# Optimization experiments

Measured on AMD Instinct MI355X. Metric: run time of the kernel, lower is better.

The kernel has to match this reference:

```python
import jax, jax.numpy as jnp
import numpy as np

B, T, C, H = 4, 4096, 1024, 64  # batch, seq, n_embd, head_size

def setup_inputs() -> dict:
    key = jax.random.key(0)
    kx, kq, kk, kv = jax.random.split(key, 4)
    x = jax.random.normal(kx, (B, T, C), dtype=jnp.float32)
    s = 1.0 / np.sqrt(C)
    Wq = jax.random.normal(kq, (C, H), dtype=jnp.float32) * s
    Wk = jax.random.normal(kk, (C, H), dtype=jnp.float32) * s
    Wv = jax.random.normal(kv, (C, H), dtype=jnp.float32) * s
    return {"x": x, "Wq": Wq, "Wk": Wk, "Wv": Wv}

def reference(x, Wq, Wk, Wv):
    B_, T_, C_ = x.shape
    q = x @ Wq  # [B,T,H]
    k = x @ Wk
    v = x @ Wv
    # NOTE: original scales by C**-0.5 (n_embd), not head_size**-0.5
    scale = jnp.asarray(C_, x.dtype) ** -0.5
    wei = jnp.einsum('bth,bsh->bts', q, k) * scale  # [B,T,T]
    causal = jnp.tril(jnp.ones((T_, T_), dtype=bool))
    wei = jnp.where(causal, wei, -jnp.inf)
    wei = jax.nn.softmax(wei, axis=-1)
    out = jnp.einsum('bts,bsh->bth', wei, v)  # [B,T,H]
    return out
```

## Files before the change

### kernel.cpp

```cpp
#include <hip/hip_runtime.h>
#include <hip/hip_bf16.h>
#include <math.h>

#define BB 4
#define TT 4096
#define CC 1024
#define HH 64

typedef __attribute__((ext_vector_type(8))) short short8;
typedef __attribute__((ext_vector_type(8))) unsigned short ushort8;
typedef __attribute__((ext_vector_type(4))) float f32x4;
typedef __attribute__((ext_vector_type(2))) unsigned int uint2v;
typedef __attribute__((ext_vector_type(4))) unsigned int uint4v;

__device__ inline unsigned short f2bf(float f) {
    unsigned int u = __builtin_bit_cast(unsigned int, f);
    unsigned int r = u + 0x7fffu + ((u >> 16) & 1u);
    return (unsigned short)(r >> 16);
}

__device__ inline unsigned int cvtpk(float lo, float hi) {
    unsigned int r;
    asm("v_cvt_pk_bf16_f32 %0, %1, %2" : "=v"(r) : "v"(lo), "v"(hi));
    return r;
}

__device__ inline float exp2v(float x) {
    float r;
    asm("v_exp_f32 %0, %1" : "=v"(r) : "v"(x));
    return r;
}

__device__ inline void gll16(const void* g, void* l) {
    __builtin_amdgcn_global_load_lds(
        (const __attribute__((address_space(1))) unsigned int*)g,
        (__attribute__((address_space(3))) unsigned int*)l,
        16, 0, 0);
}

__device__ inline int soff_strip(int qs) {
    if (qs < 128) return (qs - 64) * 2;
    if (qs < 192) return 128 + (qs - 128) * 3;
    return 320 + (qs - 192) * 4;
}

__global__ __launch_bounds__(256) void wtrans_kernel(
    const float* __restrict__ Wq,
    const float* __restrict__ Wk,
    const float* __restrict__ Wv,
    unsigned short* __restrict__ Wf)
{
    const int t = blockIdx.x * 256 + threadIdx.x;
    const int lane = t & 63;
    const int ntl  = (t >> 6) % 12;
    const int kt   = t / 768;
    const int quad = lane >> 4, n = lane & 15;
    const int m    = ntl >> 2;
    const int col  = (ntl & 3) * 16 + n;
    const float* src = (m == 0) ? Wq : (m == 1) ? Wk : Wv;
    ushort8 u;
#pragma unroll
    for (int j = 0; j < 8; ++j)
        u[j] = f2bf(src[(kt * 32 + quad * 8 + j) * 64 + col]);
    *(ushort8*)(Wf + (size_t)t * 8) = u;
}

__global__ __launch_bounds__(512, 2) void qkv_gemm(
    const float* __restrict__ x,
    const unsigned short* __restrict__ Wf,
    unsigned short* __restrict__ Qb,
    unsigned short* __restrict__ Kf,
    unsigned short* __restrict__ Vf)
{
    __shared__ __align__(16) unsigned char smem[122880];
    float (*Tl)[200] = (float (*)[200])smem;

    const int tid  = threadIdx.x;
    const int lane = tid & 63;
    const int wave = tid >> 6;
    const int n    = lane & 15;
    const int quad = lane >> 4;
    const int mt   = wave & 3;
    const int ch   = wave >> 2;

    const int row0g = blockIdx.x * 64;
    const int b     = row0g >> 12;
    const int st    = (row0g & (TT - 1)) >> 6;

    const char* xg = (const char*)(x + (size_t)row0g * CC);
    const char* wg = (const char*)Wf;

    f32x4 acc[6];
#pragma unroll
    for (int i = 0; i < 6; ++i) acc[i] = (f32x4){0.f, 0.f, 0.f, 0.f};

    auto stage = [&](int bb, int s) {
        unsigned char* base = smem + bb * 40960;
#pragma unroll
        for (int i = 0; i < 2; ++i) {
            const int rr = (i * 8 + wave) * 4 + (lane >> 4);
            const int cb = ((lane & 15) * 16) ^ ((rr & 7) << 4);
            gll16(xg + (size_t)rr * 4096 + s * 256 + cb,
                  base + (i * 8 + wave) * 1024);
        }
#pragma unroll
        for (int i = 0; i < 3; ++i) {
            const int off = (i * 8 + wave) * 1024;
            gll16(wg + (size_t)s * 24576 + off + lane * 16,
                  base + 16384 + off);
        }
    };

    auto compute = [&](int bb) {
        const unsigned char* xb = smem + bb * 40960;
        const unsigned char* wb = xb + 16384;
        const int row = mt * 16 + n;
        const int swz = (n & 7) << 4;
#pragma unroll
        for (int ktl = 0; ktl < 2; ++ktl) {
            const int c0 = (ktl * 128 + quad * 32) ^ swz;
            const int c1 = (ktl * 128 + quad * 32 + 16) ^ swz;
            const float4 f0 = *(const float4*)(xb + row * 256 + c0);
            const float4 f1 = *(const float4*)(xb + row * 256 + c1);
            uint4v u;
            u[0] = cvtpk(f0.x, f0.y);
            u[1] = cvtpk(f0.z, f0.w);
            u[2] = cvtpk(f1.x, f1.y);
            u[3] = cvtpk(f1.z, f1.w);
            const short8 a0 = __builtin_bit_cast(short8, u);
#pragma unroll
            for (int t = 0; t < 6; ++t) {
                const int g = ch * 6 + t;
                const short8 bwv = *(const short8*)(wb + (ktl * 12 + g) * 1024 + lane * 16);
                acc[t] = __builtin_amdgcn_mfma_f32_16x16x32_bf16(a0, bwv, acc[t], 0, 0, 0);
            }
        }
    };

    stage(0, 0);
    stage(1, 1);
#pragma unroll
    for (int s = 0; s < 16; ++s) {
        if (s + 2 < 16) stage((s + 2) % 3, s + 2);
        if (s <= 13)      asm volatile("s_waitcnt vmcnt(10)" ::: "memory");
        else if (s == 14) asm volatile("s_waitcnt vmcnt(5)"  ::: "memory");
        else              asm volatile("s_waitcnt vmcnt(0)"  ::: "memory");
        __builtin_amdgcn_sched_barrier(0);
        __builtin_amdgcn_s_barrier();
        compute(s % 3);
        __builtin_amdgcn_s_barrier();
    }

#pragma unroll
    for (int t = 0; t < 6; ++t) {
        const int g   = ch * 6 + t;
        const int col = (g >> 2) * 64 + (g & 3) * 16 + n;
#pragma unroll
        for (int r = 0; r < 4; ++r)
            Tl[mt * 16 + quad * 4 + r][col] = acc[t][r];
    }
    __syncthreads();

    {
        const int row = tid & 63;
        const int c0  = (tid >> 6) * 8;
        const float qsc = 0.045084220f;
        uint4v w4;
        w4[0] = cvtpk(Tl[row][c0]     * qsc, Tl[row][c0 + 1] * qsc);
        w4[1] = cvtpk(Tl[row][c0 + 2] * qsc, Tl[row][c0 + 3] * qsc);
        w4[2] = cvtpk(Tl[row][c0 + 4] * qsc, Tl[row][c0 + 5] * qsc);
        w4[3] = cvtpk(Tl[row][c0 + 6] * qsc, Tl[row][c0 + 7] * qsc);
        *(uint4v*)(Qb + (size_t)(row0g + row) * HH + c0) = w4;
    }
    {
        const int mt2 = wave >> 1, kk = wave & 1;
        ushort8 u;
#pragma unroll
        for (int j = 0; j < 8; ++j)
            u[j] = f2bf(Tl[mt2 * 16 + n][64 + kk * 32 + quad * 8 + j]);
        const size_t r = (size_t)(((b * 64 + st) * 4 + mt2) * 2 + kk) * 64 + lane;
        *(ushort8*)(Kf + r * 8) = u;
    }
    {
        const int ht = wave >> 1, kv = wave & 1;
        ushort8 u;
#pragma unroll
        for (int j = 0; j < 8; ++j)
            u[j] = f2bf(Tl[kv * 32 + quad * 8 + j][128 + ht * 16 + n]);
        const size_t r = (size_t)(((b * 64 + st) * 4 + ht) * 2 + kv) * 64 + lane;
        *(ushort8*)(Vf + r * 8) = u;
    }
}

__global__ __launch_bounds__(256) void attn_kernel(
    const unsigned short* __restrict__ Qb,
    const unsigned short* __restrict__ Kf,
    const unsigned short* __restrict__ Vf,
    float* __restrict__ out,
    float* __restrict__ scr)
{
    __shared__ unsigned short Ps[4][2][16][76];

    const int tid  = threadIdx.x;
    const int lane = tid & 63;
    const int wave = tid >> 6;
    const int n    = lane & 15;
    const int quad = lane >> 4;

    const int wid = blockIdx.x * 4 + wave;
    const int b   = wid / 640;
    const int u   = 639 - (wid - b * 640);

    int qs, ci;
    if (u < 64)        { qs = u;                  ci = 0; }
    else if (u < 192)  { const int v = u - 64;  qs = 64  + (v >> 1); ci = v & 1; }
    else if (u < 384)  { const int v = u - 192; const int d = v / 3;
                         qs = 128 + d;            ci = v - 3 * d; }
    else               { const int v = u - 384; qs = 192 + (v >> 2); ci = v & 3; }

    const int stmax = qs >> 2;
    const int st0   = ci << 4;
    const int stEnd = min(stmax, st0 + 15);
    const int nc    = (stmax + 16) >> 4;
    const int qrow  = qs * 16 + n;

    const unsigned short* qp = Qb + ((size_t)b * TT + qrow) * HH;
    const short8 bQ0 = *(const short8*)(qp + quad * 8);
    const short8 bQ1 = *(const short8*)(qp + 32 + quad * 8);

    const unsigned short* KfB = Kf + (size_t)b * 262144;
    const unsigned short* VfB = Vf + (size_t)b * 262144;

    f32x4 O[4];
#pragma unroll
    for (int ht = 0; ht < 4; ++ht) O[ht] = (f32x4){0.f, 0.f, 0.f, 0.f};
    float l = 0.f;

    short8 kA[4], kB[4];
#pragma unroll
    for (int mt = 0; mt < 4; ++mt) {
        const unsigned short* kp = KfB + (size_t)((st0 * 4 + mt) * 2) * 512 + lane * 8;
        kA[mt] = *(const short8*)(kp);
        kB[mt] = *(const short8*)(kp + 512);
    }

    for (int st = st0; st <= stEnd; ++st) {
        f32x4 S[4];
#pragma unroll
        for (int mt = 0; mt < 4; ++mt) {
            f32x4 acc = (f32x4){0.f, 0.f, 0.f, 0.f};
            acc = __builtin_amdgcn_mfma_f32_16x16x32_bf16(kA[mt], bQ0, acc, 0, 0, 0);
            acc = __builtin_amdgcn_mfma_f32_16x16x32_bf16(kB[mt], bQ1, acc, 0, 0, 0);
            S[mt] = acc;
        }

        short8 vA[4], vB[4];
#pragma unroll
        for (int ht = 0; ht < 4; ++ht) {
            const unsigned short* vp = VfB + (size_t)((st * 4 + ht) * 2) * 512 + lane * 8;
            vA[ht] = *(const short8*)(vp);
            vB[ht] = *(const short8*)(vp + 512);
        }
        if (st < stEnd) {
#pragma unroll
            for (int mt = 0; mt < 4; ++mt) {
                const unsigned short* kp = KfB + (size_t)(((st + 1) * 4 + mt) * 2) * 512 + lane * 8;
                kA[mt] = *(const short8*)(kp);
                kB[mt] = *(const short8*)(kp + 512);
            }
        }

        if (st == stmax) {
#pragma unroll
            for (int mt = 0; mt < 4; ++mt) {
                const int sg = st * 64 + mt * 16 + quad * 4;
#pragma unroll
                for (int r = 0; r < 4; ++r)
                    if (sg + r > qrow) S[mt][r] = -INFINITY;
            }
        }

#pragma unroll
        for (int mt = 0; mt < 4; ++mt)
#pragma unroll
            for (int r = 0; r < 4; ++r) {
                const float p = exp2v(fminf(S[mt][r], 43.28085f));
                S[mt][r] = p;
                l += p;
            }

        const int pp = st & 1;
#pragma unroll
        for (int mt = 0; mt < 4; ++mt) {
            uint2v w;
            w[0] = cvtpk(S[mt][0], S[mt][1]);
            w[1] = cvtpk(S[mt][2], S[mt][3]);
            *(uint2v*)&Ps[wave][pp][n][mt * 16 + quad * 4] = w;
        }
        asm volatile("s_waitcnt lgkmcnt(0)" ::: "memory");
        const short8 bP0 = *(const short8*)&Ps[wave][pp][n][quad * 8];
        const short8 bP1 = *(const short8*)&Ps[wave][pp][n][32 + quad * 8];

#pragma unroll
        for (int ht = 0; ht < 4; ++ht) {
            O[ht] = __builtin_amdgcn_mfma_f32_16x16x32_bf16(vA[ht], bP0, O[ht], 0, 0, 0);
            O[ht] = __builtin_amdgcn_mfma_f32_16x16x32_bf16(vB[ht], bP1, O[ht], 0, 0, 0);
        }
    }

    l += __shfl_xor(l, 16);
    l += __shfl_xor(l, 32);

    if (nc == 1) {
        const float inv = 1.0f / l;
        float* op = out + ((size_t)b * TT + qrow) * HH;
#pragma unroll
        for (int ht = 0; ht < 4; ++ht) {
            float4 o4;
            o4.x = O[ht][0] * inv;
            o4.y = O[ht][1] * inv;
            o4.z = O[ht][2] * inv;
            o4.w = O[ht][3] * inv;
            *(float4*)(op + ht * 16 + quad * 4) = o4;
        }
    } else {
        float* sb = scr + (size_t)(b * 576 + soff_strip(qs) + ci) * 1040;
        float* rp = sb + n * 64;
#pragma unroll
        for (int ht = 0; ht < 4; ++ht)
            *(f32x4*)(rp + ht * 16 + quad * 4) = O[ht];
        if (quad == 0) sb[1024 + n] = l;
    }
}

__global__ __launch_bounds__(64) void combine_kernel(
    const float* __restrict__ scr,
    float* __restrict__ out)
{
    const int b  = blockIdx.x / 192;
    const int qs = 64 + blockIdx.x % 192;
    const int nc = ((qs >> 2) + 16) >> 4;
    const int base = b * 576 + soff_strip(qs);

    const int t    = threadIdx.x;
    const int row  = t >> 2;
    const int col0 = (t & 3) * 16;

    f32x4 s0 = (f32x4){0.f,0.f,0.f,0.f}, s1 = s0, s2 = s0, s3 = s0;
    float lsum = 0.f;
    for (int ci = 0; ci < nc; ++ci) {
        const float* sb = scr + (size_t)(base + ci) * 1040;
        lsum += sb[1024 + row];
        const float* p = sb + row * 64 + col0;
        s0 += *(const f32x4*)(p);
        s1 += *(const f32x4*)(p + 4);
        s2 += *(const f32x4*)(p + 8);
        s3 += *(const f32x4*)(p + 12);
    }
    const float inv = 1.0f / lsum;
    float* op = out + ((size_t)b * TT + qs * 16 + row) * HH + col0;
    *(f32x4*)(op)      = s0 * inv;
    *(f32x4*)(op + 4)  = s1 * inv;
    *(f32x4*)(op + 8)  = s2 * inv;
    *(f32x4*)(op + 12) = s3 * inv;
}

extern "C" void kernel_launch(void* const* d_in, const int* in_sizes, int n_in,
                              void* d_out, int out_size, void* d_ws, size_t ws_size,
                              hipStream_t stream)
{
    const float* x  = (const float*)d_in[0];
    const float* Wq = (const float*)d_in[1];
    const float* Wk = (const float*)d_in[2];
    const float* Wv = (const float*)d_in[3];

    unsigned short* Qb = (unsigned short*)d_ws;
    unsigned short* Wf = Qb + (size_t)BB * TT * HH;
    unsigned short* Kf = Wf + (size_t)192 * 1024;
    unsigned short* Vf = Kf + (size_t)BB * 262144;
    float*          scr = (float*)(Vf + (size_t)BB * 262144);
    float* out = (float*)d_out;

    wtrans_kernel<<<96, 256, 0, stream>>>(Wq, Wk, Wv, Wf);
    qkv_gemm<<<BB * TT / 64, 512, 0, stream>>>(x, Wf, Qb, Kf, Vf);
    attn_kernel<<<640, 256, 0, stream>>>(Qb, Kf, Vf, out, scr);
    combine_kernel<<<768, 64, 0, stream>>>(scr, out);
}
```

Measured before the change: 145.6 us.

## Software-pipeline PV MFMA of previous tile with QK and softmax of current tile

```diff
diff --git a/kernel.cpp b/kernel.cpp
--- a/kernel.cpp
+++ b/kernel.cpp
@@ -243,9 +243,9 @@
         kA[mt] = *(const short8*)(kp);
         kB[mt] = *(const short8*)(kp + 512);
     }
-
-    for (int st = st0; st <= stEnd; ++st) {
-        f32x4 S[4];
+    short8 vA[4], vB[4];
+
+    auto qk_mask_softmax_write = [&](int st, f32x4* S) {
 #pragma unroll
         for (int mt = 0; mt < 4; ++mt) {
             f32x4 acc = (f32x4){0.f, 0.f, 0.f, 0.f};
@@ -253,8 +253,13 @@
             acc = __builtin_amdgcn_mfma_f32_16x16x32_bf16(kB[mt], bQ1, acc, 0, 0, 0);
             S[mt] = acc;
         }
-
-        short8 vA[4], vB[4];
+    };
+
+    {
+        const int st = st0;
+        f32x4 S[4];
+        qk_mask_softmax_write(st, S);
+
 #pragma unroll
         for (int ht = 0; ht < 4; ++ht) {
             const unsigned short* vp = VfB + (size_t)((st * 4 + ht) * 2) * 512 + lane * 8;
@@ -269,7 +274,6 @@
                 kB[mt] = *(const short8*)(kp + 512);
             }
         }
-
         if (st == stmax) {
 #pragma unroll
             for (int mt = 0; mt < 4; ++mt) {
@@ -279,7 +283,6 @@
                     if (sg + r > qrow) S[mt][r] = -INFINITY;
             }
         }
-
 #pragma unroll
         for (int mt = 0; mt < 4; ++mt)
 #pragma unroll
@@ -288,7 +291,6 @@
                 S[mt][r] = p;
                 l += p;
             }
-
         const int pp = st & 1;
 #pragma unroll
         for (int mt = 0; mt < 4; ++mt) {
@@ -297,10 +299,68 @@
             w[1] = cvtpk(S[mt][2], S[mt][3]);
             *(uint2v*)&Ps[wave][pp][n][mt * 16 + quad * 4] = w;
         }
-        asm volatile("s_waitcnt lgkmcnt(0)" ::: "memory");
-        const short8 bP0 = *(const short8*)&Ps[wave][pp][n][quad * 8];
-        const short8 bP1 = *(const short8*)&Ps[wave][pp][n][32 + quad * 8];
-
+    }
+
+    for (int st = st0 + 1; st <= stEnd; ++st) {
+        const unsigned short* prow = &Ps[wave][(st - 1) & 1][n][0];
+        const short8 bP0 = *(const short8*)(prow + quad * 8);
+        const short8 bP1 = *(const short8*)(prow + 32 + quad * 8);
+
+        f32x4 S[4];
+        qk_mask_softmax_write(st, S);
+
+#pragma unroll
+        for (int ht = 0; ht < 4; ++ht) {
+            O[ht] = __builtin_amdgcn_mfma_f32_16x16x32_bf16(vA[ht], bP0, O[ht], 0, 0, 0);
+            O[ht] = __builtin_amdgcn_mfma_f32_16x16x32_bf16(vB[ht], bP1, O[ht], 0, 0, 0);
+        }
+
+#pragma unroll
+        for (int ht = 0; ht < 4; ++ht) {
+            const unsigned short* vp = VfB + (size_t)((st * 4 + ht) * 2) * 512 + lane * 8;
+            vA[ht] = *(const short8*)(vp);
+            vB[ht] = *(const short8*)(vp + 512);
+        }
+        if (st < stEnd) {
+#pragma unroll
+            for (int mt = 0; mt < 4; ++mt) {
+                const unsigned short* kp = KfB + (size_t)(((st + 1) * 4 + mt) * 2) * 512 + lane * 8;
+                kA[mt] = *(const short8*)(kp);
+                kB[mt] = *(const short8*)(kp + 512);
+            }
+        }
+
+        if (st == stmax) {
+#pragma unroll
+            for (int mt = 0; mt < 4; ++mt) {
+                const int sg = st * 64 + mt * 16 + quad * 4;
+#pragma unroll
+                for (int r = 0; r < 4; ++r)
+                    if (sg + r > qrow) S[mt][r] = -INFINITY;
+            }
+        }
+#pragma unroll
+        for (int mt = 0; mt < 4; ++mt)
+#pragma unroll
+            for (int r = 0; r < 4; ++r) {
+                const float p = exp2v(fminf(S[mt][r], 43.28085f));
+                S[mt][r] = p;
+                l += p;
+            }
+        const int pp = st & 1;
+#pragma unroll
+        for (int mt = 0; mt < 4; ++mt) {
+            uint2v w;
+            w[0] = cvtpk(S[mt][0], S[mt][1]);
+            w[1] = cvtpk(S[mt][2], S[mt][3]);
+            *(uint2v*)&Ps[wave][pp][n][mt * 16 + quad * 4] = w;
+        }
+    }
+
+    {
+        const unsigned short* prow = &Ps[wave][stEnd & 1][n][0];
+        const short8 bP0 = *(const short8*)(prow + quad * 8);
+        const short8 bP1 = *(const short8*)(prow + 32 + quad * 8);
 #pragma unroll
         for (int ht = 0; ht < 4; ++ht) {
             O[ht] = __builtin_amdgcn_mfma_f32_16x16x32_bf16(vA[ht], bP0, O[ht], 0, 0, 0);
```

New measurement: 144.5 us. No clear change (-0.7%).

## Share K/V tiles across block waves via LDS double buffering with software-pipelined PV

Applied to the files above, without the earlier changes.

```diff
diff --git a/kernel.cpp b/kernel.cpp
--- a/kernel.cpp
+++ b/kernel.cpp
@@ -199,6 +199,7 @@
     float* __restrict__ out,
     float* __restrict__ scr)
 {
+    __shared__ __align__(16) unsigned char kv[32768];
     __shared__ unsigned short Ps[4][2][16][76];
 
     const int tid  = threadIdx.x;
@@ -207,44 +208,76 @@
     const int n    = lane & 15;
     const int quad = lane >> 4;
 
-    const int wid = blockIdx.x * 4 + wave;
-    const int b   = wid / 640;
-    const int u   = 639 - (wid - b * 640);
-
-    int qs, ci;
-    if (u < 64)        { qs = u;                  ci = 0; }
-    else if (u < 192)  { const int v = u - 64;  qs = 64  + (v >> 1); ci = v & 1; }
-    else if (u < 384)  { const int v = u - 192; const int d = v / 3;
-                         qs = 128 + d;            ci = v - 3 * d; }
-    else               { const int v = u - 384; qs = 192 + (v >> 2); ci = v & 3; }
-
-    const int stmax = qs >> 2;
+    const int bid = blockIdx.x;
+    const int b   = bid / 160;
+    const int u   = 159 - (bid - b * 160);
+
+    int g, ci;
+    if (u < 16)       { g = u;                 ci = 0; }
+    else if (u < 48)  { const int v = u - 16;  g = 16 + (v >> 1); ci = v & 1; }
+    else if (u < 96)  { const int v = u - 48;  const int d = v / 3;
+                        g = 32 + d;            ci = v - 3 * d; }
+    else              { const int v = u - 96;  g = 48 + (v >> 2); ci = v & 3; }
+
+    const int stmax = g;
     const int st0   = ci << 4;
     const int stEnd = min(stmax, st0 + 15);
     const int nc    = (stmax + 16) >> 4;
+    const int qs    = 4 * g + wave;
     const int qrow  = qs * 16 + n;
 
     const unsigned short* qp = Qb + ((size_t)b * TT + qrow) * HH;
     const short8 bQ0 = *(const short8*)(qp + quad * 8);
     const short8 bQ1 = *(const short8*)(qp + 32 + quad * 8);
 
-    const unsigned short* KfB = Kf + (size_t)b * 262144;
-    const unsigned short* VfB = Vf + (size_t)b * 262144;
+    const char* KfB = (const char*)(Kf + (size_t)b * 262144);
+    const char* VfB = (const char*)(Vf + (size_t)b * 262144);
+
+    auto stageKV = [&](int bb, int s) {
+        unsigned char* base = kv + bb * 16384 + (wave >> 1) * 8192 + (wave & 1) * 4096;
+        const char* src = ((wave >> 1) ? VfB : KfB) + (size_t)s * 8192 + (wave & 1) * 4096;
+#pragma unroll
+        for (int i = 0; i < 4; ++i)
+            gll16(src + i * 1024 + lane * 16, base + i * 1024);
+    };
 
     f32x4 O[4];
 #pragma unroll
     for (int ht = 0; ht < 4; ++ht) O[ht] = (f32x4){0.f, 0.f, 0.f, 0.f};
     float l = 0.f;
-
-    short8 kA[4], kB[4];
-#pragma unroll
-    for (int mt = 0; mt < 4; ++mt) {
-        const unsigned short* kp = KfB + (size_t)((st0 * 4 + mt) * 2) * 512 + lane * 8;
-        kA[mt] = *(const short8*)(kp);
-        kB[mt] = *(const short8*)(kp + 512);
-    }
+    short8 vA[4], vB[4];
+
+    stageKV(st0 & 1, st0);
+    asm volatile("s_waitcnt vmcnt(0)" ::: "memory");
+    __builtin_amdgcn_sched_barrier(0);
+    __builtin_amdgcn_s_barrier();
 
     for (int st = st0; st <= stEnd; ++st) {
+        const unsigned char* buf = kv + (st & 1) * 16384;
+
+        if (st < stEnd) {
+            stageKV((st + 1) & 1, st + 1);
+            asm volatile("s_waitcnt vmcnt(4)" ::: "memory");
+        } else {
+            asm volatile("s_waitcnt vmcnt(0)" ::: "memory");
+        }
+        __builtin_amdgcn_sched_barrier(0);
+        __builtin_amdgcn_s_barrier();
+
+        short8 bP0, bP1;
+        if (st > st0) {
+            const unsigned short* prow = &Ps[wave][(st - 1) & 1][n][0];
+            bP0 = *(const short8*)(prow + quad * 8);
+            bP1 = *(const short8*)(prow + 32 + quad * 8);
+        }
+
+        short8 kA[4], kB[4];
+#pragma unroll
+        for (int mt = 0; mt < 4; ++mt) {
+            kA[mt] = *(const short8*)(buf + (mt * 2 + 0) * 1024 + lane * 16);
+            kB[mt] = *(const short8*)(buf + (mt * 2 + 1) * 1024 + lane * 16);
+        }
+
         f32x4 S[4];
 #pragma unroll
         for (int mt = 0; mt < 4; ++mt) {
@@ -254,20 +287,18 @@
             S[mt] = acc;
         }
 
-        short8 vA[4], vB[4];
+        if (st > st0) {
+#pragma unroll
+            for (int ht = 0; ht < 4; ++ht) {
+                O[ht] = __builtin_amdgcn_mfma_f32_16x16x32_bf16(vA[ht], bP0, O[ht], 0, 0, 0);
+                O[ht] = __builtin_amdgcn_mfma_f32_16x16x32_bf16(vB[ht], bP1, O[ht], 0, 0, 0);
+            }
+        }
+
 #pragma unroll
         for (int ht = 0; ht < 4; ++ht) {
-            const unsigned short* vp = VfB + (size_t)((st * 4 + ht) * 2) * 512 + lane * 8;
-            vA[ht] = *(const short8*)(vp);
-            vB[ht] = *(const short8*)(vp + 512);
-        }
-        if (st < stEnd) {
-#pragma unroll
-            for (int mt = 0; mt < 4; ++mt) {
-                const unsigned short* kp = KfB + (size_t)(((st + 1) * 4 + mt) * 2) * 512 + lane * 8;
-                kA[mt] = *(const short8*)(kp);
-                kB[mt] = *(const short8*)(kp + 512);
-            }
+            vA[ht] = *(const short8*)(buf + 8192 + (ht * 2 + 0) * 1024 + lane * 16);
+            vB[ht] = *(const short8*)(buf + 8192 + (ht * 2 + 1) * 1024 + lane * 16);
         }
 
         if (st == stmax) {
@@ -297,10 +328,14 @@
             w[1] = cvtpk(S[mt][2], S[mt][3]);
             *(uint2v*)&Ps[wave][pp][n][mt * 16 + quad * 4] = w;
         }
-        asm volatile("s_waitcnt lgkmcnt(0)" ::: "memory");
-        const short8 bP0 = *(const short8*)&Ps[wave][pp][n][quad * 8];
-        const short8 bP1 = *(const short8*)&Ps[wave][pp][n][32 + quad * 8];
-
+
+        __builtin_amdgcn_s_barrier();
+    }
+
+    {
+        const unsigned short* prow = &Ps[wave][stEnd & 1][n][0];
+        const short8 bP0 = *(const short8*)(prow + quad * 8);
+        const short8 bP1 = *(const short8*)(prow + 32 + quad * 8);
 #pragma unroll
         for (int ht = 0; ht < 4; ++ht) {
             O[ht] = __builtin_amdgcn_mfma_f32_16x16x32_bf16(vA[ht], bP0, O[ht], 0, 0, 0);
```

Measured after the change: 151.4 us. 1.04x slower.
